# Kernel optimization log

Measured on AMD Instinct MI355X. Metric: run time of the kernel, lower is better.

The kernel has to match this reference:

```python
import jax, jax.numpy as jnp
import numpy as np

B, CIN, COUT, H, W, K, G = 2, 256, 256, 128, 128, 3, 4
PAD = (K - 1) // 2


def setup_inputs() -> dict:
    key = jax.random.key(0)
    k1, k2, k3, k4 = jax.random.split(key, 4)
    x = jax.random.normal(k1, (B, CIN, H, W), dtype=jnp.float32)
    # conv_offset: 1x1 conv, out channels = G*2*K*K. (Zero-init in the module; use
    # small random weights so offsets are non-trivial for correctness testing.)
    w_offset = jax.random.normal(k2, (G * 2 * K * K, CIN), dtype=jnp.float32) * 0.01
    b_offset = jax.random.normal(k3, (G * 2 * K * K,), dtype=jnp.float32) * 0.5
    # DeformConv weight (bias=False in mmcv DeformConv)
    w_deform = jax.random.normal(k4, (COUT, CIN, K, K), dtype=jnp.float32) * (1.0 / np.sqrt(CIN * K * K))
    return {"x": x, "w_offset": w_offset, "b_offset": b_offset, "w_deform": w_deform}


def _bilinear_gather(img, y, x):
    """img: [B,G,Cg,H,W]; y,x: [B,G,H,W] float sample coords -> [B,G,Cg,H,W].
    Zero padding outside the image (mmcv DCN bilinear semantics)."""
    b, g, cg, h, w = img.shape
    imgf = img.reshape(b, g, cg, h * w)
    y0 = jnp.floor(y)
    x0 = jnp.floor(x)
    out = jnp.zeros((b, g, cg, h * w), img.dtype)
    for yy, xx in ((y0, x0), (y0, x0 + 1.0), (y0 + 1.0, x0), (y0 + 1.0, x0 + 1.0)):
        wgt = (1.0 - jnp.abs(y - yy)) * (1.0 - jnp.abs(x - xx))
        valid = (yy >= 0) & (yy < h) & (xx >= 0) & (xx < w)
        wgt = jnp.where(valid, wgt, 0.0)
        yi = jnp.clip(yy, 0, h - 1).astype(jnp.int32)
        xi = jnp.clip(xx, 0, w - 1).astype(jnp.int32)
        idx = (yi * w + xi).reshape(b, g, 1, h * w)
        vals = jnp.take_along_axis(imgf, jnp.broadcast_to(idx, (b, g, cg, h * w)), axis=3)
        out = out + wgt.reshape(b, g, 1, h * w) * vals
    return out.reshape(b, g, cg, h, w)


def reference(x, w_offset, b_offset, w_deform):
    b, cin, h, w = x.shape
    cout, _, k, _ = w_deform.shape
    pad = (k - 1) // 2
    # 1x1 offset conv
    offset = jnp.einsum('bchw,oc->bohw', x, w_offset) + b_offset[None, :, None, None]
    g = offset.shape[1] // (2 * k * k)
    off = offset.reshape(b, g, k * k, 2, h, w)  # (dy, dx) per kernel tap, mmcv layout
    xg = x.reshape(b, g, cin // g, h, w)
    hh = jnp.arange(h, dtype=x.dtype)[:, None]
    ww = jnp.arange(w, dtype=x.dtype)[None, :]
    out = jnp.zeros((b, cout, h, w), x.dtype)
    for i in range(k):
        for j in range(k):
            t = i * k + j
            ys = hh - pad + i + off[:, :, t, 0]  # [B,G,H,W]
            xs = ww - pad + j + off[:, :, t, 1]
            samp = _bilinear_gather(xg, ys, xs).reshape(b, cin, h, w)
            out = out + jnp.einsum('bchw,oc->bohw', samp, w_deform[:, :, i, j])
    return jax.nn.relu(out)
```

## Files before the change

### kernel.cpp

```cpp
#include <hip/hip_runtime.h>
#include <stdint.h>

#define HW    16384
#define CIN   256
#define COUT  256
#define Hh    128
#define Ww    128
#define OFFC  72

typedef __attribute__((ext_vector_type(4))) float    f32x4;
typedef __attribute__((ext_vector_type(2))) _Float16 f16x2;
typedef __attribute__((ext_vector_type(8))) _Float16 f16x8;
typedef unsigned short u16;
typedef unsigned int   u32;

__device__ __forceinline__ u16 f2h(float f) { return __builtin_bit_cast(u16, (_Float16)f); }
__device__ __forceinline__ u32 pk2(float f) { u32 h = f2h(f); return h | (h << 16); }
__device__ __forceinline__ f16x2 bch(u32 u) { return __builtin_bit_cast(f16x2, u); }

__global__ __launch_bounds__(256) void kprep(const float* __restrict__ x, const float* __restrict__ wd,
                                             const float* __restrict__ wo, u16* __restrict__ xt,
                                             u16* __restrict__ wfrag, u16* __restrict__ wfrag2) {
  __shared__ float smem[8 * 576];
  int blk = blockIdx.x;
  if (blk < 2048) {
    int bg = blk >> 8;
    int p0 = (blk & 255) << 6;
    int pq = threadIdx.x & 15;
    int cs = threadIdx.x >> 4;
    const float* src = x + (size_t)bg * 64 * HW + p0 + pq * 4;
    u32* lds = (u32*)smem;
    #pragma unroll
    for (int s = 0; s < 2; ++s) {
      int c2 = cs + 16 * s;
      f32x4 lo = *(const f32x4*)(src + (size_t)(2 * c2 + 0) * HW);
      f32x4 hi = *(const f32x4*)(src + (size_t)(2 * c2 + 1) * HW);
      #pragma unroll
      for (int j = 0; j < 4; ++j) {
        int px = pq * 4 + j;
        u32 pkv = (u32)f2h(lo[j]) | ((u32)f2h(hi[j]) << 16);
        lds[px * 36 + ((c2 + px) & 31)] = pkv;
      }
    }
    __syncthreads();
    u16* dstb = xt + ((size_t)bg * HW + p0) * 64;
    #pragma unroll
    for (int r = 0; r < 2; ++r) {
      int e  = r * 256 + threadIdx.x;
      int px = e >> 3, c4 = e & 7;
      u32 w[4];
      #pragma unroll
      for (int m = 0; m < 4; ++m)
        w[m] = lds[px * 36 + ((4 * c4 + m + px) & 31)];
      *(uint4*)(dstb + (size_t)e * 8) = make_uint4(w[0], w[1], w[2], w[3]);
    }
  } else if (blk < 2176) {
    int bb = blk - 2048;
    int nh = bb & 31;
    int g  = bb >> 5;
    const float* src = wd + (size_t)(nh * 8) * 2304 + (size_t)g * 64 * 9;
    #pragma unroll
    for (int r = 0; r < 18; ++r) {
      int idx = threadIdx.x + 256 * r;
      int cl  = idx / 576;
      int rem = idx - cl * 576;
      smem[cl * 576 + rem] = src[(size_t)cl * 2304 + rem];
    }
    __syncthreads();
    int nt = nh >> 1, nb = (nh & 1) * 8;
    #pragma unroll
    for (int r = 0; r < 18; ++r) {
      int o  = threadIdx.x + 256 * r;
      int j  = o & 7;
      int n8 = (o >> 3) & 7;
      int q  = (o >> 6) & 3;
      int kcl = o >> 8;
      int t = kcl >> 1, half = kcl & 1;
      int cg = half * 32 + q * 8 + j;
      float v = smem[n8 * 576 + cg * 9 + t];
      int kc = (g * 9 + t) * 2 + half;
      int lane = q * 16 + nb + n8;
      wfrag[((size_t)(kc * 16 + nt) * 64 + lane) * 8 + j] = f2h(v);
    }
  } else {
    int e = (blk - 2176) * 256 + threadIdx.x;
    int j = e & 7;
    int lane = (e >> 3) & 63;
    int idx = e >> 9;
    int kc = idx / 5, nt = idx - 5 * kc;
    int n16 = lane & 15, q = lane >> 4;
    int oc = nt * 16 + n16;
    int c  = kc * 32 + q * 8 + j;
    float v = (oc < OFFC) ? wo[(size_t)oc * CIN + c] : 0.f;
    wfrag2[e] = f2h(v);
  }
}

__device__ __forceinline__ void mkpre(float yy, float xx, int* ob, u32* wp) {
  float y0f = floorf(yy), x0f = floorf(xx);
  float fy = yy - y0f, fx = xx - x0f;
  int y0 = (int)y0f, x0 = (int)x0f;
  int y1 = y0 + 1, x1 = x0 + 1;
  float vy0 = (y0 >= 0 && y0 < Hh) ? 1.f : 0.f;
  float vy1 = (y1 >= 0 && y1 < Hh) ? 1.f : 0.f;
  float vx0 = (x0 >= 0 && x0 < Ww) ? 1.f : 0.f;
  float vx1 = (x1 >= 0 && x1 < Ww) ? 1.f : 0.f;
  wp[0] = pk2((1.f - fy) * (1.f - fx) * vy0 * vx0);
  wp[1] = pk2((1.f - fy) * fx * vy0 * vx1);
  wp[2] = pk2(fy * (1.f - fx) * vy1 * vx0);
  wp[3] = pk2(fy * fx * vy1 * vx1);
  int cy0 = min(max(y0, 0), Hh - 1), cy1 = min(max(y1, 0), Hh - 1);
  int cx0 = min(max(x0, 0), Ww - 1), cx1 = min(max(x1, 0), Ww - 1);
  ob[0] = (cy0 * Ww + cx0) << 7;
  ob[1] = (cy0 * Ww + cx1) << 7;
  ob[2] = (cy1 * Ww + cx0) << 7;
  ob[3] = (cy1 * Ww + cx1) << 7;
}

__device__ __forceinline__ uint4 bil16(const uint4* v, const u32* wp) {
  f16x2 W0 = bch(wp[0]), W1 = bch(wp[1]), W2 = bch(wp[2]), W3 = bch(wp[3]);
  uint4 r;
  { f16x2 s = bch(v[0].x) * W0 + bch(v[1].x) * W1 + bch(v[2].x) * W2 + bch(v[3].x) * W3; r.x = __builtin_bit_cast(u32, s); }
  { f16x2 s = bch(v[0].y) * W0 + bch(v[1].y) * W1 + bch(v[2].y) * W2 + bch(v[3].y) * W3; r.y = __builtin_bit_cast(u32, s); }
  { f16x2 s = bch(v[0].z) * W0 + bch(v[1].z) * W1 + bch(v[2].z) * W2 + bch(v[3].z) * W3; r.z = __builtin_bit_cast(u32, s); }
  { f16x2 s = bch(v[0].w) * W0 + bch(v[1].w) * W1 + bch(v[2].w) * W2 + bch(v[3].w) * W3; r.w = __builtin_bit_cast(u32, s); }
  return r;
}

__global__ __launch_bounds__(512) void k2(const u16* __restrict__ xt, const u16* __restrict__ wfrag2,
                                          const float* __restrict__ bo, const u16* __restrict__ wfrag,
                                          float* __restrict__ out) {
  __shared__ u16   astage[2 * 8 * 512];
  __shared__ float offl[64 * 74];
  int tid  = threadIdx.x;
  int lane = tid & 63, n16 = lane & 15, q = (tid >> 4) & 3;
  int wv   = tid >> 6;
  int sp   = wv >> 1;
  int hp   = wv & 1;
  int blk  = blockIdx.x;
  int swz  = (blk & 7) * 64 + (blk >> 3);
  int b  = swz >> 8;
  int p0 = (swz & 255) << 6;
  int h  = p0 >> 7, w0 = p0 & 127;
  const char* xtb = (const char*)xt + (size_t)b * 4 * HW * 128;
  float fh  = (float)h;
  float fxp = (float)(w0 + sp * 16 + n16);
  int   chb = hp * 64 + q * 16;

  f32x4 acc[4][2];
  #pragma unroll
  for (int mt = 0; mt < 4; ++mt) {
    acc[mt][0] = (f32x4){0.f, 0.f, 0.f, 0.f};
    acc[mt][1] = (f32x4){0.f, 0.f, 0.f, 0.f};
  }

  if (wv < 4) {
    f32x4 oacc[5];
    #pragma unroll
    for (int nt = 0; nt < 5; ++nt) {
      int oc = nt * 16 + n16;
      float bv = (oc < OFFC) ? bo[oc] : 0.f;
      oacc[nt] = (f32x4){bv, bv, bv, bv};
    }
    #pragma unroll
    for (int kc = 0; kc < 8; ++kc) {
      int g = kc >> 1;
      f16x8 af = __builtin_bit_cast(f16x8, *(const uint4*)(xtb +
          ((size_t)(g * HW + p0 + wv * 16 + n16)) * 128 + (kc & 1) * 64 + q * 16));
      #pragma unroll
      for (int nt = 0; nt < 5; ++nt) {
        f16x8 bfo = __builtin_bit_cast(f16x8, *(const uint4*)(wfrag2 + (size_t)(((kc * 5 + nt) << 6) + lane) * 8));
        oacc[nt] = __builtin_amdgcn_mfma_f32_16x16x32_f16(af, bfo, oacc[nt], 0, 0, 0);
      }
    }
    #pragma unroll
    for (int nt = 0; nt < 5; ++nt) {
      int oc = nt * 16 + n16;
      if (oc < OFFC) {
        #pragma unroll
        for (int r = 0; r < 4; ++r)
          offl[(wv * 16 + q * 4 + r) * 74 + oc] = oacc[nt][r];
      }
    }
  }
  uint4 bf0[2];
  bf0[0] = *(const uint4*)(wfrag + ((size_t)(wv * 2 + 0) * 64 + lane) * 8);
  bf0[1] = *(const uint4*)(wfrag + ((size_t)(wv * 2 + 1) * 64 + lane) * 8);
  __syncthreads();

  uint4 dA[4], dB[4];
  u32   wpA[4], wpB[4];

  auto issue = [&](int gt, uint4* dd, u32* wpp) {
    int pxl = sp * 16 + n16;
    float oy = offl[pxl * 74 + gt * 2];
    float ox = offl[pxl * 74 + gt * 2 + 1];
    int g = (gt * 57) >> 9;
    int t = gt - g * 9;
    int i = (t * 683) >> 11;
    int j = t - i * 3;
    int ob[4];
    mkpre(fh + (float)(i - 1) + oy, fxp + (float)(j - 1) + ox, ob, wpp);
    const char* xg = xtb + (size_t)g * HW * 128;
    #pragma unroll
    for (int c = 0; c < 4; ++c)
      dd[c] = *(const uint4*)(xg + ob[c] + chb);
  };
  auto consume = [&](int slot, int gt) {
    uint4 bf1[2];
    const u16* wb1 = wfrag + ((size_t)((2 * gt + 1) * 16 + wv * 2) * 64 + lane) * 8;
    bf1[0] = *(const uint4*)(wb1);
    bf1[1] = *(const uint4*)(wb1 + 512);
    #pragma unroll
    for (int mt = 0; mt < 4; ++mt) {
      f16x8 af = __builtin_bit_cast(f16x8,
          *(const uint4*)&astage[(slot * 8 + mt * 2 + 0) * 512 + lane * 8]);
      acc[mt][0] = __builtin_amdgcn_mfma_f32_16x16x32_f16(af, __builtin_bit_cast(f16x8, bf0[0]), acc[mt][0], 0, 0, 0);
      acc[mt][1] = __builtin_amdgcn_mfma_f32_16x16x32_f16(af, __builtin_bit_cast(f16x8, bf0[1]), acc[mt][1], 0, 0, 0);
    }
    #pragma unroll
    for (int mt = 0; mt < 4; ++mt) {
      f16x8 af = __builtin_bit_cast(f16x8,
          *(const uint4*)&astage[(slot * 8 + mt * 2 + 1) * 512 + lane * 8]);
      acc[mt][0] = __builtin_amdgcn_mfma_f32_16x16x32_f16(af, __builtin_bit_cast(f16x8, bf1[0]), acc[mt][0], 0, 0, 0);
      acc[mt][1] = __builtin_amdgcn_mfma_f32_16x16x32_f16(af, __builtin_bit_cast(f16x8, bf1[1]), acc[mt][1], 0, 0, 0);
    }
    if (gt < 35) {
      const u16* wb0 = wfrag + ((size_t)((2 * gt + 2) * 16 + wv * 2) * 64 + lane) * 8;
      bf0[0] = *(const uint4*)(wb0);
      bf0[1] = *(const uint4*)(wb0 + 512);
    }
  };

  issue(0, dA, wpA);
  issue(1, dB, wpB);
  *(uint4*)&astage[(0 * 8 + sp * 2 + hp) * 512 + lane * 8] = bil16(dA, wpA);
  __syncthreads();

  #pragma unroll 1
  for (int gt = 0; gt < 36; gt += 2) {
    *(uint4*)&astage[(1 * 8 + sp * 2 + hp) * 512 + lane * 8] = bil16(dB, wpB);
    if (gt + 2 < 36) issue(gt + 2, dA, wpA);
    consume(0, gt);
    __syncthreads();
    if (gt + 2 < 36) {
      *(uint4*)&astage[(0 * 8 + sp * 2 + hp) * 512 + lane * 8] = bil16(dA, wpA);
      issue(gt + 3, dB, wpB);
    }
    consume(1, gt + 1);
    __syncthreads();
  }

  float* op = out + (size_t)b * COUT * HW + p0;
  #pragma unroll
  for (int mt = 0; mt < 4; ++mt)
    #pragma unroll
    for (int j = 0; j < 2; ++j) {
      f32x4 v = acc[mt][j];
      #pragma unroll
      for (int r = 0; r < 4; ++r) v[r] = fmaxf(v[r], 0.f);
      int cout = wv * 32 + j * 16 + n16;
      *(f32x4*)(op + (size_t)cout * HW + mt * 16 + q * 4) = v;
    }
}

extern "C" void kernel_launch(void* const* d_in, const int* in_sizes, int n_in,
                              void* d_out, int out_size, void* d_ws, size_t ws_size,
                              hipStream_t stream) {
  const float* x  = (const float*)d_in[0];
  const float* wo = (const float*)d_in[1];
  const float* bo = (const float*)d_in[2];
  const float* wd = (const float*)d_in[3];
  float* out = (float*)d_out;

  u16* xtp    = (u16*)d_ws;
  u16* wfrag  = (u16*)((char*)d_ws + 16777216);
  u16* wfrag2 = (u16*)((char*)d_ws + 16777216 + 1179648);

  kprep<<<2256, 256, 0, stream>>>(x, wd, wo, xtp, wfrag, wfrag2);
  k2   <<<512,  512, 0, stream>>>(xtp, wfrag2, bo, wfrag, out);
}
```

Measured before the change: 178.2 us.

## Process two deformable taps per stage with four LDS slots to halve barriers

```diff
diff --git a/kernel.cpp b/kernel.cpp
--- a/kernel.cpp
+++ b/kernel.cpp
@@ -127,10 +127,10 @@
   return r;
 }
 
-__global__ __launch_bounds__(512) void k2(const u16* __restrict__ xt, const u16* __restrict__ wfrag2,
-                                          const float* __restrict__ bo, const u16* __restrict__ wfrag,
-                                          float* __restrict__ out) {
-  __shared__ u16   astage[2 * 8 * 512];
+__global__ __launch_bounds__(512, 4) void k2(const u16* __restrict__ xt, const u16* __restrict__ wfrag2,
+                                             const float* __restrict__ bo, const u16* __restrict__ wfrag,
+                                             float* __restrict__ out) {
+  __shared__ u16   astage[2 * 2 * 8 * 512];
   __shared__ float offl[64 * 74];
   int tid  = threadIdx.x;
   int lane = tid & 63, n16 = lane & 15, q = (tid >> 4) & 3;
@@ -146,6 +146,7 @@
   float fh  = (float)h;
   float fxp = (float)(w0 + sp * 16 + n16);
   int   chb = hp * 64 + q * 16;
+  int   pxl = sp * 16 + n16;
 
   f32x4 acc[4][2];
   #pragma unroll
@@ -183,16 +184,17 @@
       }
     }
   }
-  uint4 bf0[2];
-  bf0[0] = *(const uint4*)(wfrag + ((size_t)(wv * 2 + 0) * 64 + lane) * 8);
-  bf0[1] = *(const uint4*)(wfrag + ((size_t)(wv * 2 + 1) * 64 + lane) * 8);
+  uint4 bf0E[2], bf0O[2];
+  bf0E[0] = *(const uint4*)(wfrag + ((size_t)(0 * 16 + wv * 2 + 0) * 64 + lane) * 8);
+  bf0E[1] = *(const uint4*)(wfrag + ((size_t)(0 * 16 + wv * 2 + 1) * 64 + lane) * 8);
+  bf0O[0] = *(const uint4*)(wfrag + ((size_t)(2 * 16 + wv * 2 + 0) * 64 + lane) * 8);
+  bf0O[1] = *(const uint4*)(wfrag + ((size_t)(2 * 16 + wv * 2 + 1) * 64 + lane) * 8);
   __syncthreads();
 
-  uint4 dA[4], dB[4];
-  u32   wpA[4], wpB[4];
-
-  auto issue = [&](int gt, uint4* dd, u32* wpp) {
-    int pxl = sp * 16 + n16;
+  uint4 dT0[4], dT1[4];
+  u32   wpT0[4], wpT1[4];
+
+  auto issue1 = [&](int gt, uint4* dd, u32* wpp) {
     float oy = offl[pxl * 74 + gt * 2];
     float ox = offl[pxl * 74 + gt * 2 + 1];
     int g = (gt * 57) >> 9;
@@ -206,7 +208,7 @@
     for (int c = 0; c < 4; ++c)
       dd[c] = *(const uint4*)(xg + ob[c] + chb);
   };
-  auto consume = [&](int slot, int gt) {
+  auto consume = [&](int slot, int gt, uint4* bf0s) {
     uint4 bf1[2];
     const u16* wb1 = wfrag + ((size_t)((2 * gt + 1) * 16 + wv * 2) * 64 + lane) * 8;
     bf1[0] = *(const uint4*)(wb1);
@@ -215,8 +217,8 @@
     for (int mt = 0; mt < 4; ++mt) {
       f16x8 af = __builtin_bit_cast(f16x8,
           *(const uint4*)&astage[(slot * 8 + mt * 2 + 0) * 512 + lane * 8]);
-      acc[mt][0] = __builtin_amdgcn_mfma_f32_16x16x32_f16(af, __builtin_bit_cast(f16x8, bf0[0]), acc[mt][0], 0, 0, 0);
-      acc[mt][1] = __builtin_amdgcn_mfma_f32_16x16x32_f16(af, __builtin_bit_cast(f16x8, bf0[1]), acc[mt][1], 0, 0, 0);
+      acc[mt][0] = __builtin_amdgcn_mfma_f32_16x16x32_f16(af, __builtin_bit_cast(f16x8, bf0s[0]), acc[mt][0], 0, 0, 0);
+      acc[mt][1] = __builtin_amdgcn_mfma_f32_16x16x32_f16(af, __builtin_bit_cast(f16x8, bf0s[1]), acc[mt][1], 0, 0, 0);
     }
     #pragma unroll
     for (int mt = 0; mt < 4; ++mt) {
@@ -225,29 +227,38 @@
       acc[mt][0] = __builtin_amdgcn_mfma_f32_16x16x32_f16(af, __builtin_bit_cast(f16x8, bf1[0]), acc[mt][0], 0, 0, 0);
       acc[mt][1] = __builtin_amdgcn_mfma_f32_16x16x32_f16(af, __builtin_bit_cast(f16x8, bf1[1]), acc[mt][1], 0, 0, 0);
     }
-    if (gt < 35) {
-      const u16* wb0 = wfrag + ((size_t)((2 * gt + 2) * 16 + wv * 2) * 64 + lane) * 8;
-      bf0[0] = *(const uint4*)(wb0);
-      bf0[1] = *(const uint4*)(wb0 + 512);
+    if (gt + 2 < 36) {
+      const u16* wb0 = wfrag + ((size_t)((2 * (gt + 2)) * 16 + wv * 2) * 64 + lane) * 8;
+      bf0s[0] = *(const uint4*)(wb0);
+      bf0s[1] = *(const uint4*)(wb0 + 512);
     }
   };
 
-  issue(0, dA, wpA);
-  issue(1, dB, wpB);
-  *(uint4*)&astage[(0 * 8 + sp * 2 + hp) * 512 + lane * 8] = bil16(dA, wpA);
+  issue1(0, dT0, wpT0);
+  issue1(1, dT1, wpT1);
+  *(uint4*)&astage[((0 * 2 + 0) * 8 + wv) * 512 + lane * 8] = bil16(dT0, wpT0);
+  *(uint4*)&astage[((0 * 2 + 1) * 8 + wv) * 512 + lane * 8] = bil16(dT1, wpT1);
   __syncthreads();
 
   #pragma unroll 1
-  for (int gt = 0; gt < 36; gt += 2) {
-    *(uint4*)&astage[(1 * 8 + sp * 2 + hp) * 512 + lane * 8] = bil16(dB, wpB);
-    if (gt + 2 < 36) issue(gt + 2, dA, wpA);
-    consume(0, gt);
-    __syncthreads();
-    if (gt + 2 < 36) {
-      *(uint4*)&astage[(0 * 8 + sp * 2 + hp) * 512 + lane * 8] = bil16(dA, wpA);
-      issue(gt + 3, dB, wpB);
-    }
-    consume(1, gt + 1);
+  for (int s = 0; s < 18; s += 2) {
+    issue1(2 * s + 2, dT0, wpT0);
+    issue1(2 * s + 3, dT1, wpT1);
+    consume(0, 2 * s,     bf0E);
+    consume(1, 2 * s + 1, bf0O);
+    *(uint4*)&astage[((1 * 2 + 0) * 8 + wv) * 512 + lane * 8] = bil16(dT0, wpT0);
+    *(uint4*)&astage[((1 * 2 + 1) * 8 + wv) * 512 + lane * 8] = bil16(dT1, wpT1);
+    __syncthreads();
+    if (s + 2 < 18) {
+      issue1(2 * s + 4, dT0, wpT0);
+      issue1(2 * s + 5, dT1, wpT1);
+    }
+    consume(2, 2 * s + 2, bf0E);
+    consume(3, 2 * s + 3, bf0O);
+    if (s + 2 < 18) {
+      *(uint4*)&astage[((0 * 2 + 0) * 8 + wv) * 512 + lane * 8] = bil16(dT0, wpT0);
+      *(uint4*)&astage[((0 * 2 + 1) * 8 + wv) * 512 + lane * 8] = bil16(dT1, wpT1);
+    }
     __syncthreads();
   }
 
```

Result: no change. 179.5 us (+0.8%).

## Double k2 tile to a full 128-pixel row with 16 waves per block

Applied to the files above, without the earlier changes.

```diff
diff --git a/kernel.cpp b/kernel.cpp
--- a/kernel.cpp
+++ b/kernel.cpp
@@ -127,34 +127,32 @@
   return r;
 }
 
-__global__ __launch_bounds__(512) void k2(const u16* __restrict__ xt, const u16* __restrict__ wfrag2,
-                                          const float* __restrict__ bo, const u16* __restrict__ wfrag,
-                                          float* __restrict__ out) {
-  __shared__ u16   astage[2 * 8 * 512];
-  __shared__ float offl[64 * 74];
+__global__ __launch_bounds__(1024, 4) void k2(const u16* __restrict__ xt, const u16* __restrict__ wfrag2,
+                                              const float* __restrict__ bo, const u16* __restrict__ wfrag,
+                                              float* __restrict__ out) {
+  __shared__ u16   astage[2 * 16 * 512];
+  __shared__ float offl[128 * 74];
   int tid  = threadIdx.x;
   int lane = tid & 63, n16 = lane & 15, q = (tid >> 4) & 3;
   int wv   = tid >> 6;
   int sp   = wv >> 1;
   int hp   = wv & 1;
   int blk  = blockIdx.x;
-  int swz  = (blk & 7) * 64 + (blk >> 3);
-  int b  = swz >> 8;
-  int p0 = (swz & 255) << 6;
-  int h  = p0 >> 7, w0 = p0 & 127;
+  int swz  = (blk & 7) * 32 + (blk >> 3);
+  int b  = swz >> 7;
+  int p0 = (swz & 127) << 7;
+  int h  = p0 >> 7;
   const char* xtb = (const char*)xt + (size_t)b * 4 * HW * 128;
   float fh  = (float)h;
-  float fxp = (float)(w0 + sp * 16 + n16);
+  float fxp = (float)(sp * 16 + n16);
   int   chb = hp * 64 + q * 16;
-
-  f32x4 acc[4][2];
+  int   pxl = sp * 16 + n16;
+
+  f32x4 acc[8];
   #pragma unroll
-  for (int mt = 0; mt < 4; ++mt) {
-    acc[mt][0] = (f32x4){0.f, 0.f, 0.f, 0.f};
-    acc[mt][1] = (f32x4){0.f, 0.f, 0.f, 0.f};
-  }
-
-  if (wv < 4) {
+  for (int mt = 0; mt < 8; ++mt) acc[mt] = (f32x4){0.f, 0.f, 0.f, 0.f};
+
+  if (wv < 8) {
     f32x4 oacc[5];
     #pragma unroll
     for (int nt = 0; nt < 5; ++nt) {
@@ -183,16 +181,21 @@
       }
     }
   }
-  uint4 bf0[2];
-  bf0[0] = *(const uint4*)(wfrag + ((size_t)(wv * 2 + 0) * 64 + lane) * 8);
-  bf0[1] = *(const uint4*)(wfrag + ((size_t)(wv * 2 + 1) * 64 + lane) * 8);
-  __syncthreads();
 
   uint4 dA[4], dB[4];
   u32   wpA[4], wpB[4];
+  uint4 bfA[2], bfB[2];
+
+  auto bfld = [&](int gt, uint4* bf) {
+    const u16* wb = wfrag + ((size_t)((2 * gt) * 16 + wv) * 64 + lane) * 8;
+    bf[0] = *(const uint4*)(wb);
+    bf[1] = *(const uint4*)(wb + 8192);
+  };
+
+  bfld(0, bfA);
+  __syncthreads();
 
   auto issue = [&](int gt, uint4* dd, u32* wpp) {
-    int pxl = sp * 16 + n16;
     float oy = offl[pxl * 74 + gt * 2];
     float ox = offl[pxl * 74 + gt * 2 + 1];
     int g = (gt * 57) >> 9;
@@ -206,62 +209,48 @@
     for (int c = 0; c < 4; ++c)
       dd[c] = *(const uint4*)(xg + ob[c] + chb);
   };
-  auto consume = [&](int slot, int gt) {
-    uint4 bf1[2];
-    const u16* wb1 = wfrag + ((size_t)((2 * gt + 1) * 16 + wv * 2) * 64 + lane) * 8;
-    bf1[0] = *(const uint4*)(wb1);
-    bf1[1] = *(const uint4*)(wb1 + 512);
-    #pragma unroll
-    for (int mt = 0; mt < 4; ++mt) {
-      f16x8 af = __builtin_bit_cast(f16x8,
-          *(const uint4*)&astage[(slot * 8 + mt * 2 + 0) * 512 + lane * 8]);
-      acc[mt][0] = __builtin_amdgcn_mfma_f32_16x16x32_f16(af, __builtin_bit_cast(f16x8, bf0[0]), acc[mt][0], 0, 0, 0);
-      acc[mt][1] = __builtin_amdgcn_mfma_f32_16x16x32_f16(af, __builtin_bit_cast(f16x8, bf0[1]), acc[mt][1], 0, 0, 0);
-    }
-    #pragma unroll
-    for (int mt = 0; mt < 4; ++mt) {
-      f16x8 af = __builtin_bit_cast(f16x8,
-          *(const uint4*)&astage[(slot * 8 + mt * 2 + 1) * 512 + lane * 8]);
-      acc[mt][0] = __builtin_amdgcn_mfma_f32_16x16x32_f16(af, __builtin_bit_cast(f16x8, bf1[0]), acc[mt][0], 0, 0, 0);
-      acc[mt][1] = __builtin_amdgcn_mfma_f32_16x16x32_f16(af, __builtin_bit_cast(f16x8, bf1[1]), acc[mt][1], 0, 0, 0);
-    }
-    if (gt < 35) {
-      const u16* wb0 = wfrag + ((size_t)((2 * gt + 2) * 16 + wv * 2) * 64 + lane) * 8;
-      bf0[0] = *(const uint4*)(wb0);
-      bf0[1] = *(const uint4*)(wb0 + 512);
+  auto consume = [&](int slot, uint4* bf) {
+    #pragma unroll
+    for (int mt = 0; mt < 8; ++mt) {
+      f16x8 af0 = __builtin_bit_cast(f16x8,
+          *(const uint4*)&astage[(slot * 16 + mt * 2 + 0) * 512 + lane * 8]);
+      acc[mt] = __builtin_amdgcn_mfma_f32_16x16x32_f16(af0, __builtin_bit_cast(f16x8, bf[0]), acc[mt], 0, 0, 0);
+      f16x8 af1 = __builtin_bit_cast(f16x8,
+          *(const uint4*)&astage[(slot * 16 + mt * 2 + 1) * 512 + lane * 8]);
+      acc[mt] = __builtin_amdgcn_mfma_f32_16x16x32_f16(af1, __builtin_bit_cast(f16x8, bf[1]), acc[mt], 0, 0, 0);
     }
   };
 
   issue(0, dA, wpA);
   issue(1, dB, wpB);
-  *(uint4*)&astage[(0 * 8 + sp * 2 + hp) * 512 + lane * 8] = bil16(dA, wpA);
+  *(uint4*)&astage[(0 * 16 + sp * 2 + hp) * 512 + lane * 8] = bil16(dA, wpA);
   __syncthreads();
 
   #pragma unroll 1
   for (int gt = 0; gt < 36; gt += 2) {
-    *(uint4*)&astage[(1 * 8 + sp * 2 + hp) * 512 + lane * 8] = bil16(dB, wpB);
+    *(uint4*)&astage[(1 * 16 + sp * 2 + hp) * 512 + lane * 8] = bil16(dB, wpB);
+    bfld(gt + 1, bfB);
     if (gt + 2 < 36) issue(gt + 2, dA, wpA);
-    consume(0, gt);
+    consume(0, bfA);
     __syncthreads();
     if (gt + 2 < 36) {
-      *(uint4*)&astage[(0 * 8 + sp * 2 + hp) * 512 + lane * 8] = bil16(dA, wpA);
+      *(uint4*)&astage[(0 * 16 + sp * 2 + hp) * 512 + lane * 8] = bil16(dA, wpA);
+      bfld(gt + 2, bfA);
       issue(gt + 3, dB, wpB);
     }
-    consume(1, gt + 1);
+    consume(1, bfB);
     __syncthreads();
   }
 
   float* op = out + (size_t)b * COUT * HW + p0;
+  int cout = wv * 16 + n16;
   #pragma unroll
-  for (int mt = 0; mt < 4; ++mt)
-    #pragma unroll
-    for (int j = 0; j < 2; ++j) {
-      f32x4 v = acc[mt][j];
-      #pragma unroll
-      for (int r = 0; r < 4; ++r) v[r] = fmaxf(v[r], 0.f);
-      int cout = wv * 32 + j * 16 + n16;
-      *(f32x4*)(op + (size_t)cout * HW + mt * 16 + q * 4) = v;
-    }
+  for (int mt = 0; mt < 8; ++mt) {
+    f32x4 v = acc[mt];
+    #pragma unroll
+    for (int r = 0; r < 4; ++r) v[r] = fmaxf(v[r], 0.f);
+    *(f32x4*)(op + (size_t)cout * HW + mt * 16 + q * 4) = v;
+  }
 }
 
 extern "C" void kernel_launch(void* const* d_in, const int* in_sizes, int n_in,
@@ -278,5 +267,5 @@
   u16* wfrag2 = (u16*)((char*)d_ws + 16777216 + 1179648);
 
   kprep<<<2256, 256, 0, stream>>>(x, wd, wo, xtp, wfrag, wfrag2);
-  k2   <<<512,  512, 0, stream>>>(xtp, wfrag2, bo, wfrag, out);
-}
+  k2   <<<256, 1024, 0, stream>>>(xtp, wfrag2, bo, wfrag, out);
+}
```

After: 176.0 us (median of 2 runs). Within noise of the previous version (-1.2%).
